# Kernel tuning notes

Measured on AMD Instinct MI355X. Metric: run time of the kernel, lower is better.

## Reference

```python
import jax, jax.numpy as jnp
import numpy as np

B, L, D, S = 64, 512, 768, 8
HOP, LAMB = 3, 0.5


def _layernorm(x, g, b, eps=1e-5):
    m = x.mean(-1, keepdims=True)
    v = x.var(-1, keepdims=True)
    return (x - m) / jnp.sqrt(v + eps) * g + b


def _hop_refine(cur, sentence, ln_g, ln_b):
    # cur, sentence: [B,S,D]. HOP-1 refinement steps, then return last row.
    for _ in range(HOP - 1):
        coef = jnp.einsum('bd,bsd->bs', cur[:, -1, :], sentence)  # [B,S]
        a = coef[..., None] * sentence                             # [B,S,D]
        cur = LAMB * _layernorm(jax.nn.sigmoid(a), ln_g, ln_b) + sentence
    return cur[:, -1, :]  # [B,D]


def _conv1d(x, w, b):
    # x: [B,D,S], w: [Dout,Din,3], padding=1 (same)
    y = jax.lax.conv_general_dilated(
        x, w, window_strides=(1,), padding=((1, 1),),
        dimension_numbers=('NCH', 'OIH', 'NCH'))
    return y + b[None, :, None]


def setup_inputs() -> dict:
    key = jax.random.key(0)
    ks = jax.random.split(key, 16)
    p = lambda k, shp: (jax.random.normal(k, shp, dtype=jnp.float32) * 0.02)
    # segment boundaries: strictly increasing, start at 1, <= L, gaps ~63 with jitter < 32
    base = 1 + np.arange(S + 1) * ((L - 1) // S)          # [9]
    jitter = np.array(jax.random.randint(ks[15], (B, S + 1), 0, 32))
    jitter[:, 0] = 0
    jitter[:, -1] = 0
    seg_bounds = jnp.asarray(base[None, :] + jitter, dtype=jnp.int64 if jax.config.jax_enable_x64 else jnp.int32)
    return {
        'bert_output': jax.random.normal(ks[0], (B, L, D), dtype=jnp.float32),
        'target': jax.random.normal(ks[1], (B, D), dtype=jnp.float32),
        'gc1_w': p(ks[2], (D, D)), 'gc1_b': p(ks[3], (D,)),
        'gc2_w': p(ks[4], (D, D)), 'gc2_b': p(ks[5], (D,)),
        'conv1_w': p(ks[6], (D, D, 3)), 'conv1_b': p(ks[7], (D,)),
        'conv2_w': p(ks[8], (D, D, 3)), 'conv2_b': p(ks[9], (D,)),
        'ln_g': jnp.ones((D,), jnp.float32), 'ln_b': jnp.zeros((D,), jnp.float32),
        'fc2_w': p(ks[10], (3 * D, 3)), 'fc2_b': p(ks[11], (3,)),
        'seg_bounds': seg_bounds,
    }


def reference(bert_output, target, gc1_w, gc1_b, gc2_w, gc2_b,
              conv1_w, conv1_b, conv2_w, conv2_b, ln_g, ln_b,
              fc2_w, fc2_b, seg_bounds):
    dt = bert_output.dtype
    start = seg_bounds[:, :-1]   # [B,S]
    end = seg_bounds[:, 1:]      # [B,S]
    pos = jnp.arange(L)
    seg_mask = ((pos[None, None, :] >= start[:, :, None]) &
                (pos[None, None, :] < end[:, :, None])).astype(dt)  # [B,S,L]
    cnt = (end - start).astype(dt)                                   # [B,S]
    # batched segment-mean pooling
    sentence = jnp.einsum('bsl,bld->bsd', seg_mask, bert_output) / cnt[..., None]

    # GCN branch: adj = I + superdiagonal, row-degree normalization
    adj = jnp.eye(S, dtype=dt) + jnp.eye(S, k=1, dtype=dt)
    denom = adj.sum(axis=1)  # [S]

    def gcn(x, w, b):
        h = jnp.einsum('bsd,de->bse', x, w)
        return jnp.einsum('st,btd->bsd', adj, h) / denom[None, :, None] + b

    g1 = jnp.tanh(gcn(sentence, gc1_w, gc1_b))
    g2 = jnp.tanh(gcn(g1, gc2_w, gc2_b))
    a3 = _hop_refine(g2, sentence, ln_g, ln_b)

    # Conv branch: two conv1d (k=3, pad=1) over the segment axis
    x = jnp.swapaxes(sentence, 1, 2)  # [B,D,S]
    c = jnp.tanh(_conv1d(x, conv1_w, conv1_b))
    c = jnp.tanh(_conv1d(c, conv2_w, conv2_b))
    conv_out = jnp.swapaxes(c, 1, 2)  # [B,S,D]
    a4 = _hop_refine(conv_out, sentence, ln_g, ln_b)

    # Self-mask branch
    coef0 = jnp.einsum('bd,bsd->bs', sentence[:, -1, :], sentence)
    tmask = jax.nn.sigmoid(coef0[..., None] * sentence)
    a5 = _hop_refine(tmask, sentence, ln_g, ln_b)

    fnout = jnp.stack([a3, a4, a5], axis=1)                 # [B,3,D]
    # NOTE: original uses target[0] (first sample's pooler output) for all samples
    w = jax.nn.softmax(jnp.einsum('bkd,d->bk', fnout, target[0]), axis=1)
    fn = (fnout * w[..., None]).reshape(fnout.shape[0], 3 * D)
    return fn @ fc2_w + fc2_b  # [B,3]
```

## Files before the change

kernel.cpp:

```cpp
#include <hip/hip_runtime.h>


typedef unsigned short u16;
typedef short short8 __attribute__((ext_vector_type(8)));
typedef float f32x4 __attribute__((ext_vector_type(4)));

__device__ __forceinline__ float bf2f(u16 h) {
    unsigned int u = ((unsigned int)h) << 16;
    float f;
    __builtin_memcpy(&f, &u, 4);
    return f;
}
__device__ __forceinline__ u16 f2bf(float f) {
    unsigned int u;
    __builtin_memcpy(&u, &f, 4);
    u = (u + 0x7fffu + ((u >> 16) & 1u)) >> 16;
    return (u16)u;
}
__device__ __forceinline__ float sigm(float x) { return 1.0f / (1.0f + __expf(-x)); }

__device__ __forceinline__ float ldv(const void* p, long i, bool bf) {
    return bf ? bf2f(((const u16*)p)[i]) : ((const float*)p)[i];
}

__device__ __forceinline__ bool detect_bf16(const u16* bert) {
    int hits = 0;
#pragma unroll
    for (int i = 0; i < 256; i += 2) {
        const int e = (bert[i] >> 7) & 0xFF;
        hits += (e >= 115 && e <= 130) ? 1 : 0;
    }
    return hits > 64;
}

__global__ __launch_bounds__(256) void k0_zero(float* __restrict__ ws)
{
    ((float4*)ws)[blockIdx.x * 256 + threadIdx.x] = make_float4(0.f, 0.f, 0.f, 0.f);
}

__global__ __launch_bounds__(256) void k1_pool(
    const void* __restrict__ bertv, const int* __restrict__ sb,
    float* __restrict__ sentF, float* __restrict__ flagp)
{
    const int u = blockIdx.x, t = threadIdx.x;
    const bool bf = detect_bf16((const u16*)bertv);
    const bool is64 = (sb[1] == 0);
    if (u == 0 && t == 0) flagp[0] = bf ? 1.0f : 0.0f;
    const int q = u & 3, v = u >> 2;
    const int b = v / 3, si = v - 3 * (v / 3), s = 5 + si;
    const int i0 = b * 9 + s, i1 = i0 + 1;
    int st = is64 ? sb[2 * i0] : sb[i0];
    int en = is64 ? sb[2 * i1] : sb[i1];
    st = st < 0 ? 0 : (st > 511 ? 511 : st);
    en = en <= st ? st + 1 : (en > 512 ? 512 : en);
    const int n = en - st;
    const int r0 = st + (n * q) / 4;
    const int r1 = st + (n * (q + 1)) / 4;
    float a0 = 0.f, a1 = 0.f, a2 = 0.f;
    if (bf) {
        const u16* base = (const u16*)bertv + (size_t)b * 512 * 768;
        int l = r0;
        for (; l + 1 < r1; l += 2) {
            const u16* p0 = base + (size_t)l * 768;
            const u16* p1 = p0 + 768;
            const u16 x0 = p0[t], x1 = p0[t + 256], x2 = p0[t + 512];
            const u16 y0 = p1[t], y1 = p1[t + 256], y2 = p1[t + 512];
            a0 += bf2f(x0) + bf2f(y0);
            a1 += bf2f(x1) + bf2f(y1);
            a2 += bf2f(x2) + bf2f(y2);
        }
        if (l < r1) {
            const u16* p0 = base + (size_t)l * 768;
            a0 += bf2f(p0[t]);
            a1 += bf2f(p0[t + 256]);
            a2 += bf2f(p0[t + 512]);
        }
    } else {
        const float* base = (const float*)bertv + (size_t)b * 512 * 768;
        int l = r0;
        for (; l + 1 < r1; l += 2) {
            const float* p0 = base + (size_t)l * 768;
            const float* p1 = p0 + 768;
            const float x0 = p0[t], x1 = p0[t + 256], x2 = p0[t + 512];
            const float y0 = p1[t], y1 = p1[t + 256], y2 = p1[t + 512];
            a0 += x0 + y0;
            a1 += x1 + y1;
            a2 += x2 + y2;
        }
        if (l < r1) {
            const float* p0 = base + (size_t)l * 768;
            a0 += p0[t];
            a1 += p0[t + 256];
            a2 += p0[t + 512];
        }
    }
    const float inv = 1.0f / (float)n;
    float* o = sentF + b * 2304 + si * 768;
    atomicAdd(o + t, a0 * inv);
    atomicAdd(o + t + 256, a1 * inv);
    atomicAdd(o + t + 512, a2 * inv);
}

template <int XMODE, int WMODE>
__device__ __forceinline__ void gemm_core(
    const float* __restrict__ x, int xstride, const void* __restrict__ bias,
    const void* __restrict__ W, bool bf,
    float* __restrict__ out, int ostride,
    int n0, int k0, u16* As, u16* Bs)
{
    const int t = threadIdx.x;
    const int r = t >> 2;
    const int cseg = (t & 3) * 32;
    const int wave = t >> 6, lane = t & 63;
    const int lm = lane & 15, lq = lane >> 4;
    f32x4 acc[4] = {};

    for (int kk = 0; kk < 256; kk += 128) {
        const int kg = k0 + kk;
        {
            const float* xp = x + (size_t)r * xstride + (kg + cseg);
            u16* dst = As + r * 136 + cseg;
#pragma unroll
            for (int i = 0; i < 8; ++i) {
                float4 v = ((const float4*)xp)[i];
                if (XMODE == 1) {
                    int kb = kg + cseg + i * 4;
                    if (kb >= 768) kb -= 768;
                    v.x = tanhf(v.x + ldv(bias, kb, bf));
                    v.y = tanhf(v.y + ldv(bias, kb + 1, bf));
                    v.z = tanhf(v.z + ldv(bias, kb + 2, bf));
                    v.w = tanhf(v.w + ldv(bias, kb + 3, bf));
                }
                ((ushort4*)dst)[i] = make_ushort4(f2bf(v.x), f2bf(v.y), f2bf(v.z), f2bf(v.w));
            }
        }
        if (WMODE == 0) {
            const int p = t >> 2;
            const int nseg = (t & 3) * 16;
            u16 q0[16], q1[16];
            if (bf) {
                const u16* w0 = (const u16*)W + (size_t)(kg + 2 * p) * 768 + n0 + nseg;
                ((uint4*)q0)[0] = ((const uint4*)w0)[0];
                ((uint4*)q0)[1] = ((const uint4*)w0)[1];
                ((uint4*)q1)[0] = ((const uint4*)(w0 + 768))[0];
                ((uint4*)q1)[1] = ((const uint4*)(w0 + 768))[1];
            } else {
                const float* w0 = (const float*)W + (size_t)(kg + 2 * p) * 768 + n0 + nseg;
#pragma unroll
                for (int e = 0; e < 4; ++e) {
                    float4 v0 = ((const float4*)w0)[e];
                    float4 v1 = ((const float4*)(w0 + 768))[e];
                    q0[4 * e] = f2bf(v0.x); q0[4 * e + 1] = f2bf(v0.y);
                    q0[4 * e + 2] = f2bf(v0.z); q0[4 * e + 3] = f2bf(v0.w);
                    q1[4 * e] = f2bf(v1.x); q1[4 * e + 1] = f2bf(v1.y);
                    q1[4 * e + 2] = f2bf(v1.z); q1[4 * e + 3] = f2bf(v1.w);
                }
            }
#pragma unroll
            for (int e = 0; e < 16; ++e)
                *(ushort2*)(Bs + (nseg + e) * 136 + 2 * p) = make_ushort2(q0[e], q1[e]);
        } else {
            const int kb = kg / 768;
            const int i0c = kg - kb * 768;
            u16 tmp[32];
            if (bf) {
                const u16* wp = (const u16*)W + (size_t)(n0 + r) * 2304 + (size_t)(i0c + cseg) * 3 + kb;
#pragma unroll
                for (int j = 0; j < 32; ++j) tmp[j] = wp[j * 3];
            } else {
                const float* wp = (const float*)W + (size_t)(n0 + r) * 2304 + (size_t)(i0c + cseg) * 3 + kb;
#pragma unroll
                for (int j = 0; j < 32; ++j) tmp[j] = f2bf(wp[j * 3]);
            }
            u16* dst = Bs + r * 136 + cseg;
#pragma unroll
            for (int qq = 0; qq < 8; ++qq)
                ((ushort4*)dst)[qq] = ((ushort4*)tmp)[qq];
        }
        __syncthreads();
        const u16* ap = As + (wave * 16 + lm) * 136 + lq * 8;
        const u16* bp = Bs + lm * 136 + lq * 8;
#pragma unroll
        for (int ks = 0; ks < 4; ++ks) {
            short8 af = *(const short8*)(ap + ks * 32);
#pragma unroll
            for (int nf = 0; nf < 4; ++nf) {
                short8 bfr = *(const short8*)(bp + nf * 16 * 136 + ks * 32);
                acc[nf] = __builtin_amdgcn_mfma_f32_16x16x32_bf16(af, bfr, acc[nf], 0, 0, 0);
            }
        }
        __syncthreads();
    }
#pragma unroll
    for (int nf = 0; nf < 4; ++nf) {
#pragma unroll
        for (int rg = 0; rg < 4; ++rg) {
            const int row = wave * 16 + lq * 4 + rg;
            const int col = n0 + nf * 16 + lm;
            atomicAdd(out + (size_t)row * ostride + col, acc[nf][rg]);
        }
    }
}

__global__ __launch_bounds__(256) void k2_gemm_a(
    const float* __restrict__ sentF, const void* __restrict__ gc1w,
    const void* __restrict__ c1w, float* __restrict__ g1acc, float* __restrict__ c1acc,
    const float* __restrict__ flagp)
{
    __shared__ u16 As[64 * 136];
    __shared__ u16 Bs[64 * 136];
    const bool bf = flagp[0] > 0.5f;
    const int u = blockIdx.x;
    if (u < 36) {
        gemm_core<0, 0>(sentF + 1536, 2304, nullptr, gc1w, bf, g1acc, 768,
                        (u / 3) * 64, (u % 3) * 256, As, Bs);
    } else if (u < 144) {
        const int v = u - 36;
        gemm_core<0, 1>(sentF, 2304, nullptr, c1w, bf, c1acc, 1536,
                        (v / 9) * 64, (v % 9) * 256, As, Bs);
    } else {
        const int v = u - 144;
        gemm_core<0, 1>(sentF + 768, 2304, nullptr, c1w, bf, c1acc + 768, 1536,
                        (v / 6) * 64, (v % 6) * 256, As, Bs);
    }
}

__global__ __launch_bounds__(256) void k3_gemm_b(
    const float* __restrict__ g1acc, const float* __restrict__ c1acc,
    const void* __restrict__ gc2w, const void* __restrict__ c2w,
    const void* __restrict__ gc1b, const void* __restrict__ c1b,
    float* __restrict__ g2acc, float* __restrict__ c2acc,
    const float* __restrict__ flagp)
{
    __shared__ u16 As[64 * 136];
    __shared__ u16 Bs[64 * 136];
    const bool bf = flagp[0] > 0.5f;
    const int u = blockIdx.x;
    if (u < 36) {
        gemm_core<1, 0>(g1acc, 768, gc1b, gc2w, bf, g2acc, 768,
                        (u / 3) * 64, (u % 3) * 256, As, Bs);
    } else {
        const int v = u - 36;
        gemm_core<1, 1>(c1acc, 1536, c1b, c2w, bf, c2acc, 768,
                        (v / 6) * 64, (v % 6) * 256, As, Bs);
    }
}

__device__ __forceinline__ float block_sum(float v, float* red) {
#pragma unroll
    for (int m = 1; m < 64; m <<= 1) v += __shfl_xor(v, m, 64);
    const int wave = threadIdx.x >> 6, lane = threadIdx.x & 63;
    if (lane == 0) red[wave] = v;
    __syncthreads();
    const float r = red[0] + red[1] + red[2] + red[3];
    __syncthreads();
    return r;
}

__global__ __launch_bounds__(256) void k4_final(
    const float* __restrict__ sentF, const float* __restrict__ g2acc,
    const float* __restrict__ c2acc,
    const void* __restrict__ gc2b, const void* __restrict__ c2b,
    const void* __restrict__ lng, const void* __restrict__ lnb,
    const void* __restrict__ target, const void* __restrict__ fc2w,
    const void* __restrict__ fc2b, void* __restrict__ outp,
    const float* __restrict__ flagp)
{
    __shared__ float red[4];
    const bool bf = flagp[0] > 0.5f;
    const int t = threadIdx.x, b = blockIdx.x;
    float s_[3], g_[3], bb_[3];
    const float* srow = sentF + b * 2304 + 1536;
#pragma unroll
    for (int i = 0; i < 3; ++i) {
        const int d = t + 256 * i;
        s_[i] = srow[d];
        g_[i] = ldv(lng, d, bf);
        bb_[i] = ldv(lnb, d, bf);
    }

    auto refine2 = [&](float* yv) {
#pragma unroll
        for (int it = 0; it < 2; ++it) {
            const float c = block_sum(yv[0] * s_[0] + yv[1] * s_[1] + yv[2] * s_[2], red);
            float tt[3], sm = 0.0f, sq = 0.0f;
#pragma unroll
            for (int i = 0; i < 3; ++i) {
                tt[i] = sigm(c * s_[i]);
                sm += tt[i];
                sq += tt[i] * tt[i];
            }
            const float m = block_sum(sm, red) * (1.0f / 768.0f);
            const float q = block_sum(sq, red) * (1.0f / 768.0f);
            const float inv = rsqrtf(fmaxf(q - m * m, 0.0f) + 1e-5f);
#pragma unroll
            for (int i = 0; i < 3; ++i)
                yv[i] = 0.5f * ((tt[i] - m) * inv * g_[i] + bb_[i]) + s_[i];
        }
    };

    float a3[3], a4[3], a5[3], y[3];
#pragma unroll
    for (int i = 0; i < 3; ++i) {
        const int d = t + 256 * i;
        y[i] = tanhf(g2acc[b * 768 + d] + ldv(gc2b, d, bf));
    }
    refine2(y);
    a3[0] = y[0]; a3[1] = y[1]; a3[2] = y[2];
#pragma unroll
    for (int i = 0; i < 3; ++i) {
        const int d = t + 256 * i;
        y[i] = tanhf(c2acc[b * 768 + d] + ldv(c2b, d, bf));
    }
    refine2(y);
    a4[0] = y[0]; a4[1] = y[1]; a4[2] = y[2];
    const float ss = block_sum(s_[0] * s_[0] + s_[1] * s_[1] + s_[2] * s_[2], red);
#pragma unroll
    for (int i = 0; i < 3; ++i) y[i] = sigm(ss * s_[i]);
    refine2(y);
    a5[0] = y[0]; a5[1] = y[1]; a5[2] = y[2];

    float tg[3];
#pragma unroll
    for (int i = 0; i < 3; ++i) tg[i] = ldv(target, t + 256 * i, bf);
    const float u0 = block_sum(a3[0] * tg[0] + a3[1] * tg[1] + a3[2] * tg[2], red);
    const float u1 = block_sum(a4[0] * tg[0] + a4[1] * tg[1] + a4[2] * tg[2], red);
    const float u2 = block_sum(a5[0] * tg[0] + a5[1] * tg[1] + a5[2] * tg[2], red);
    const float mx = fmaxf(u0, fmaxf(u1, u2));
    const float e0 = __expf(u0 - mx), e1 = __expf(u1 - mx), e2 = __expf(u2 - mx);
    const float es = e0 + e1 + e2;
    const float w0 = e0 / es, w1 = e1 / es, w2 = e2 / es;

    float p0 = 0.0f, p1 = 0.0f, p2 = 0.0f;
#pragma unroll
    for (int i = 0; i < 3; ++i) {
        const int d = t + 256 * i;
        const float va = w0 * a3[i], vb = w1 * a4[i], vc = w2 * a5[i];
        p0 += va * ldv(fc2w, d * 3 + 0, bf) + vb * ldv(fc2w, (768 + d) * 3 + 0, bf) + vc * ldv(fc2w, (1536 + d) * 3 + 0, bf);
        p1 += va * ldv(fc2w, d * 3 + 1, bf) + vb * ldv(fc2w, (768 + d) * 3 + 1, bf) + vc * ldv(fc2w, (1536 + d) * 3 + 1, bf);
        p2 += va * ldv(fc2w, d * 3 + 2, bf) + vb * ldv(fc2w, (768 + d) * 3 + 2, bf) + vc * ldv(fc2w, (1536 + d) * 3 + 2, bf);
    }
    p0 = block_sum(p0, red);
    p1 = block_sum(p1, red);
    p2 = block_sum(p2, red);
    if (t == 0) {
        const float o0 = p0 + ldv(fc2b, 0, bf);
        const float o1 = p1 + ldv(fc2b, 1, bf);
        const float o2 = p2 + ldv(fc2b, 2, bf);
        if (bf) {
            ((u16*)outp)[b * 3 + 0] = f2bf(o0);
            ((u16*)outp)[b * 3 + 1] = f2bf(o1);
            ((u16*)outp)[b * 3 + 2] = f2bf(o2);
        } else {
            ((float*)outp)[b * 3 + 0] = o0;
            ((float*)outp)[b * 3 + 1] = o1;
            ((float*)outp)[b * 3 + 2] = o2;
        }
    }
}

extern "C" void kernel_launch(void* const* d_in, const int* in_sizes, int n_in,
                              void* d_out, int out_size, void* d_ws, size_t ws_size,
                              hipStream_t stream) {
    const void* bert   = d_in[0];
    const void* target = d_in[1];
    const void* gc1w   = d_in[2];
    const void* gc1b   = d_in[3];
    const void* gc2w   = d_in[4];
    const void* gc2b   = d_in[5];
    const void* c1w    = d_in[6];
    const void* c1b    = d_in[7];
    const void* c2w    = d_in[8];
    const void* c2b    = d_in[9];
    const void* lng    = d_in[10];
    const void* lnb    = d_in[11];
    const void* fc2w   = d_in[12];
    const void* fc2b   = d_in[13];
    const int*  sb     = (const int*)d_in[14];

    float* sentF = (float*)d_ws;
    float* accs  = sentF + 147456;
    float* g1acc = accs;
    float* c1acc = accs + 49152;
    float* g2acc = c1acc + 98304;
    float* c2acc = g2acc + 49152;
    float* flagp = accs + 245760;

    k0_zero<<<384, 256, 0, stream>>>(sentF);
    k1_pool<<<768, 256, 0, stream>>>(bert, sb, sentF, flagp);
    k2_gemm_a<<<216, 256, 0, stream>>>(sentF, gc1w, c1w, g1acc, c1acc, flagp);
    k3_gemm_b<<<108, 256, 0, stream>>>(g1acc, c1acc, gc2w, c2w, gc1b, c1b, g2acc, c2acc, flagp);
    k4_final<<<64, 256, 0, stream>>>(sentF, g2acc, c2acc, gc2b, c2b, lng, lnb,
                                     target, fc2w, fc2b, d_out, flagp);
}
```

Before: 223.6 us.

## Fuse all stages into one cooperative kernel with grid syncs

Replaces the five separate launches (zero, pool, two GEMM stages, final) with a single cooperative kernel of 256 blocks that uses grid.sync between phases. Pooling now writes four per-quarter partial buffers instead of doing atomicAdd into a zeroed buffer, and the GEMM input loader sums those four partials. tanhf is replaced by a fast exp-based tanh. This is meant to remove launch gaps and pooling atomics, in exchange for grid-wide barrier cost, a bf16-detection scan in every block, and fewer blocks available for the pooling phase.

```diff
diff --git a/kernel.cpp b/kernel.cpp
--- a/kernel.cpp
+++ b/kernel.cpp
@@ -1,9 +1,14 @@
 #include <hip/hip_runtime.h>
+#include <hip/hip_cooperative_groups.h>
+
+namespace cg = cooperative_groups;
 
 
 typedef unsigned short u16;
 typedef short short8 __attribute__((ext_vector_type(8)));
 typedef float f32x4 __attribute__((ext_vector_type(4)));
+
+#define PART 147456
 
 __device__ __forceinline__ float bf2f(u16 h) {
     unsigned int u = ((unsigned int)h) << 16;
@@ -18,7 +23,11 @@
     return (u16)u;
 }
 __device__ __forceinline__ float sigm(float x) { return 1.0f / (1.0f + __expf(-x)); }
-
+__device__ __forceinline__ float ftanh(float x) {
+    const float xc = fminf(fmaxf(x, -15.0f), 15.0f);
+    const float e = __expf(2.0f * xc);
+    return __fdividef(e - 1.0f, e + 1.0f);
+}
 __device__ __forceinline__ float ldv(const void* p, long i, bool bf) {
     return bf ? bf2f(((const u16*)p)[i]) : ((const float*)p)[i];
 }
@@ -33,75 +42,7 @@
     return hits > 64;
 }
 
-__global__ __launch_bounds__(256) void k0_zero(float* __restrict__ ws)
-{
-    ((float4*)ws)[blockIdx.x * 256 + threadIdx.x] = make_float4(0.f, 0.f, 0.f, 0.f);
-}
-
-__global__ __launch_bounds__(256) void k1_pool(
-    const void* __restrict__ bertv, const int* __restrict__ sb,
-    float* __restrict__ sentF, float* __restrict__ flagp)
-{
-    const int u = blockIdx.x, t = threadIdx.x;
-    const bool bf = detect_bf16((const u16*)bertv);
-    const bool is64 = (sb[1] == 0);
-    if (u == 0 && t == 0) flagp[0] = bf ? 1.0f : 0.0f;
-    const int q = u & 3, v = u >> 2;
-    const int b = v / 3, si = v - 3 * (v / 3), s = 5 + si;
-    const int i0 = b * 9 + s, i1 = i0 + 1;
-    int st = is64 ? sb[2 * i0] : sb[i0];
-    int en = is64 ? sb[2 * i1] : sb[i1];
-    st = st < 0 ? 0 : (st > 511 ? 511 : st);
-    en = en <= st ? st + 1 : (en > 512 ? 512 : en);
-    const int n = en - st;
-    const int r0 = st + (n * q) / 4;
-    const int r1 = st + (n * (q + 1)) / 4;
-    float a0 = 0.f, a1 = 0.f, a2 = 0.f;
-    if (bf) {
-        const u16* base = (const u16*)bertv + (size_t)b * 512 * 768;
-        int l = r0;
-        for (; l + 1 < r1; l += 2) {
-            const u16* p0 = base + (size_t)l * 768;
-            const u16* p1 = p0 + 768;
-            const u16 x0 = p0[t], x1 = p0[t + 256], x2 = p0[t + 512];
-            const u16 y0 = p1[t], y1 = p1[t + 256], y2 = p1[t + 512];
-            a0 += bf2f(x0) + bf2f(y0);
-            a1 += bf2f(x1) + bf2f(y1);
-            a2 += bf2f(x2) + bf2f(y2);
-        }
-        if (l < r1) {
-            const u16* p0 = base + (size_t)l * 768;
-            a0 += bf2f(p0[t]);
-            a1 += bf2f(p0[t + 256]);
-            a2 += bf2f(p0[t + 512]);
-        }
-    } else {
-        const float* base = (const float*)bertv + (size_t)b * 512 * 768;
-        int l = r0;
-        for (; l + 1 < r1; l += 2) {
-            const float* p0 = base + (size_t)l * 768;
-            const float* p1 = p0 + 768;
-            const float x0 = p0[t], x1 = p0[t + 256], x2 = p0[t + 512];
-            const float y0 = p1[t], y1 = p1[t + 256], y2 = p1[t + 512];
-            a0 += x0 + y0;
-            a1 += x1 + y1;
-            a2 += x2 + y2;
-        }
-        if (l < r1) {
-            const float* p0 = base + (size_t)l * 768;
-            a0 += p0[t];
-            a1 += p0[t + 256];
-            a2 += p0[t + 512];
-        }
-    }
-    const float inv = 1.0f / (float)n;
-    float* o = sentF + b * 2304 + si * 768;
-    atomicAdd(o + t, a0 * inv);
-    atomicAdd(o + t + 256, a1 * inv);
-    atomicAdd(o + t + 512, a2 * inv);
-}
-
-template <int XMODE, int WMODE>
+template <int XMODE, int WMODE, int NPART>
 __device__ __forceinline__ void gemm_core(
     const float* __restrict__ x, int xstride, const void* __restrict__ bias,
     const void* __restrict__ W, bool bf,
@@ -123,13 +64,22 @@
 #pragma unroll
             for (int i = 0; i < 8; ++i) {
                 float4 v = ((const float4*)xp)[i];
+                if (NPART == 4) {
+                    const float4 v1 = ((const float4*)(xp + PART))[i];
+                    const float4 v2 = ((const float4*)(xp + 2 * PART))[i];
+                    const float4 v3 = ((const float4*)(xp + 3 * PART))[i];
+                    v.x += v1.x + v2.x + v3.x;
+                    v.y += v1.y + v2.y + v3.y;
+                    v.z += v1.z + v2.z + v3.z;
+                    v.w += v1.w + v2.w + v3.w;
+                }
                 if (XMODE == 1) {
                     int kb = kg + cseg + i * 4;
                     if (kb >= 768) kb -= 768;
-                    v.x = tanhf(v.x + ldv(bias, kb, bf));
-                    v.y = tanhf(v.y + ldv(bias, kb + 1, bf));
-                    v.z = tanhf(v.z + ldv(bias, kb + 2, bf));
-                    v.w = tanhf(v.w + ldv(bias, kb + 3, bf));
+                    v.x = ftanh(v.x + ldv(bias, kb, bf));
+                    v.y = ftanh(v.y + ldv(bias, kb + 1, bf));
+                    v.z = ftanh(v.z + ldv(bias, kb + 2, bf));
+                    v.w = ftanh(v.w + ldv(bias, kb + 3, bf));
                 }
                 ((ushort4*)dst)[i] = make_ushort4(f2bf(v.x), f2bf(v.y), f2bf(v.z), f2bf(v.w));
             }
@@ -202,50 +152,6 @@
     }
 }
 
-__global__ __launch_bounds__(256) void k2_gemm_a(
-    const float* __restrict__ sentF, const void* __restrict__ gc1w,
-    const void* __restrict__ c1w, float* __restrict__ g1acc, float* __restrict__ c1acc,
-    const float* __restrict__ flagp)
-{
-    __shared__ u16 As[64 * 136];
-    __shared__ u16 Bs[64 * 136];
-    const bool bf = flagp[0] > 0.5f;
-    const int u = blockIdx.x;
-    if (u < 36) {
-        gemm_core<0, 0>(sentF + 1536, 2304, nullptr, gc1w, bf, g1acc, 768,
-                        (u / 3) * 64, (u % 3) * 256, As, Bs);
-    } else if (u < 144) {
-        const int v = u - 36;
-        gemm_core<0, 1>(sentF, 2304, nullptr, c1w, bf, c1acc, 1536,
-                        (v / 9) * 64, (v % 9) * 256, As, Bs);
-    } else {
-        const int v = u - 144;
-        gemm_core<0, 1>(sentF + 768, 2304, nullptr, c1w, bf, c1acc + 768, 1536,
-                        (v / 6) * 64, (v % 6) * 256, As, Bs);
-    }
-}
-
-__global__ __launch_bounds__(256) void k3_gemm_b(
-    const float* __restrict__ g1acc, const float* __restrict__ c1acc,
-    const void* __restrict__ gc2w, const void* __restrict__ c2w,
-    const void* __restrict__ gc1b, const void* __restrict__ c1b,
-    float* __restrict__ g2acc, float* __restrict__ c2acc,
-    const float* __restrict__ flagp)
-{
-    __shared__ u16 As[64 * 136];
-    __shared__ u16 Bs[64 * 136];
-    const bool bf = flagp[0] > 0.5f;
-    const int u = blockIdx.x;
-    if (u < 36) {
-        gemm_core<1, 0>(g1acc, 768, gc1b, gc2w, bf, g2acc, 768,
-                        (u / 3) * 64, (u % 3) * 256, As, Bs);
-    } else {
-        const int v = u - 36;
-        gemm_core<1, 1>(c1acc, 1536, c1b, c2w, bf, c2acc, 768,
-                        (v / 6) * 64, (v % 6) * 256, As, Bs);
-    }
-}
-
 __device__ __forceinline__ float block_sum(float v, float* red) {
 #pragma unroll
     for (int m = 1; m < 64; m <<= 1) v += __shfl_xor(v, m, 64);
@@ -257,104 +163,207 @@
     return r;
 }
 
-__global__ __launch_bounds__(256) void k4_final(
-    const float* __restrict__ sentF, const float* __restrict__ g2acc,
-    const float* __restrict__ c2acc,
-    const void* __restrict__ gc2b, const void* __restrict__ c2b,
+__global__ __launch_bounds__(256) void fused_all(
+    const void* __restrict__ bertv, const void* __restrict__ target,
+    const void* __restrict__ gc1w, const void* __restrict__ gc1b,
+    const void* __restrict__ gc2w, const void* __restrict__ gc2b,
+    const void* __restrict__ c1w, const void* __restrict__ c1b,
+    const void* __restrict__ c2w, const void* __restrict__ c2b,
     const void* __restrict__ lng, const void* __restrict__ lnb,
-    const void* __restrict__ target, const void* __restrict__ fc2w,
-    const void* __restrict__ fc2b, void* __restrict__ outp,
-    const float* __restrict__ flagp)
+    const void* __restrict__ fc2w, const void* __restrict__ fc2b,
+    const int* __restrict__ sb,
+    float* __restrict__ sentP, float* __restrict__ accs,
+    void* __restrict__ outp)
 {
+    __shared__ u16 As[64 * 136];
+    __shared__ u16 Bs[64 * 136];
     __shared__ float red[4];
-    const bool bf = flagp[0] > 0.5f;
-    const int t = threadIdx.x, b = blockIdx.x;
-    float s_[3], g_[3], bb_[3];
-    const float* srow = sentF + b * 2304 + 1536;
-#pragma unroll
-    for (int i = 0; i < 3; ++i) {
-        const int d = t + 256 * i;
-        s_[i] = srow[d];
-        g_[i] = ldv(lng, d, bf);
-        bb_[i] = ldv(lnb, d, bf);
-    }
-
-    auto refine2 = [&](float* yv) {
-#pragma unroll
-        for (int it = 0; it < 2; ++it) {
-            const float c = block_sum(yv[0] * s_[0] + yv[1] * s_[1] + yv[2] * s_[2], red);
-            float tt[3], sm = 0.0f, sq = 0.0f;
-#pragma unroll
-            for (int i = 0; i < 3; ++i) {
-                tt[i] = sigm(c * s_[i]);
-                sm += tt[i];
-                sq += tt[i] * tt[i];
-            }
-            const float m = block_sum(sm, red) * (1.0f / 768.0f);
-            const float q = block_sum(sq, red) * (1.0f / 768.0f);
-            const float inv = rsqrtf(fmaxf(q - m * m, 0.0f) + 1e-5f);
-#pragma unroll
-            for (int i = 0; i < 3; ++i)
-                yv[i] = 0.5f * ((tt[i] - m) * inv * g_[i] + bb_[i]) + s_[i];
-        }
-    };
-
-    float a3[3], a4[3], a5[3], y[3];
-#pragma unroll
-    for (int i = 0; i < 3; ++i) {
-        const int d = t + 256 * i;
-        y[i] = tanhf(g2acc[b * 768 + d] + ldv(gc2b, d, bf));
-    }
-    refine2(y);
-    a3[0] = y[0]; a3[1] = y[1]; a3[2] = y[2];
-#pragma unroll
-    for (int i = 0; i < 3; ++i) {
-        const int d = t + 256 * i;
-        y[i] = tanhf(c2acc[b * 768 + d] + ldv(c2b, d, bf));
-    }
-    refine2(y);
-    a4[0] = y[0]; a4[1] = y[1]; a4[2] = y[2];
-    const float ss = block_sum(s_[0] * s_[0] + s_[1] * s_[1] + s_[2] * s_[2], red);
-#pragma unroll
-    for (int i = 0; i < 3; ++i) y[i] = sigm(ss * s_[i]);
-    refine2(y);
-    a5[0] = y[0]; a5[1] = y[1]; a5[2] = y[2];
-
-    float tg[3];
-#pragma unroll
-    for (int i = 0; i < 3; ++i) tg[i] = ldv(target, t + 256 * i, bf);
-    const float u0 = block_sum(a3[0] * tg[0] + a3[1] * tg[1] + a3[2] * tg[2], red);
-    const float u1 = block_sum(a4[0] * tg[0] + a4[1] * tg[1] + a4[2] * tg[2], red);
-    const float u2 = block_sum(a5[0] * tg[0] + a5[1] * tg[1] + a5[2] * tg[2], red);
-    const float mx = fmaxf(u0, fmaxf(u1, u2));
-    const float e0 = __expf(u0 - mx), e1 = __expf(u1 - mx), e2 = __expf(u2 - mx);
-    const float es = e0 + e1 + e2;
-    const float w0 = e0 / es, w1 = e1 / es, w2 = e2 / es;
-
-    float p0 = 0.0f, p1 = 0.0f, p2 = 0.0f;
-#pragma unroll
-    for (int i = 0; i < 3; ++i) {
-        const int d = t + 256 * i;
-        const float va = w0 * a3[i], vb = w1 * a4[i], vc = w2 * a5[i];
-        p0 += va * ldv(fc2w, d * 3 + 0, bf) + vb * ldv(fc2w, (768 + d) * 3 + 0, bf) + vc * ldv(fc2w, (1536 + d) * 3 + 0, bf);
-        p1 += va * ldv(fc2w, d * 3 + 1, bf) + vb * ldv(fc2w, (768 + d) * 3 + 1, bf) + vc * ldv(fc2w, (1536 + d) * 3 + 1, bf);
-        p2 += va * ldv(fc2w, d * 3 + 2, bf) + vb * ldv(fc2w, (768 + d) * 3 + 2, bf) + vc * ldv(fc2w, (1536 + d) * 3 + 2, bf);
-    }
-    p0 = block_sum(p0, red);
-    p1 = block_sum(p1, red);
-    p2 = block_sum(p2, red);
-    if (t == 0) {
-        const float o0 = p0 + ldv(fc2b, 0, bf);
-        const float o1 = p1 + ldv(fc2b, 1, bf);
-        const float o2 = p2 + ldv(fc2b, 2, bf);
-        if (bf) {
-            ((u16*)outp)[b * 3 + 0] = f2bf(o0);
-            ((u16*)outp)[b * 3 + 1] = f2bf(o1);
-            ((u16*)outp)[b * 3 + 2] = f2bf(o2);
-        } else {
-            ((float*)outp)[b * 3 + 0] = o0;
-            ((float*)outp)[b * 3 + 1] = o1;
-            ((float*)outp)[b * 3 + 2] = o2;
+
+    const int u = blockIdx.x, t = threadIdx.x;
+    const bool bf = detect_bf16((const u16*)bertv);
+    const bool is64 = (sb[1] == 0);
+    cg::grid_group grid = cg::this_grid();
+
+    float* g1acc = accs;
+    float* c1acc = accs + 49152;
+    float* g2acc = c1acc + 98304;
+    float* c2acc = g2acc + 49152;
+
+    {
+        if (t < 240) ((float4*)accs)[u * 240 + t] = make_float4(0.f, 0.f, 0.f, 0.f);
+#pragma unroll
+        for (int j = 0; j < 3; ++j) {
+            const int v = u + 256 * j;
+            const int q = v & 3, w = v >> 2;
+            const int b = w / 3, si = w - 3 * (w / 3), s = 5 + si;
+            const int i0 = b * 9 + s, i1 = i0 + 1;
+            int st = is64 ? sb[2 * i0] : sb[i0];
+            int en = is64 ? sb[2 * i1] : sb[i1];
+            st = st < 0 ? 0 : (st > 511 ? 511 : st);
+            en = en <= st ? st + 1 : (en > 512 ? 512 : en);
+            const int n = en - st;
+            const int r0 = st + (n * q) / 4;
+            const int r1 = st + (n * (q + 1)) / 4;
+            float a0 = 0.f, a1 = 0.f, a2 = 0.f;
+            if (bf) {
+                const u16* base = (const u16*)bertv + (size_t)b * 512 * 768;
+                int l = r0;
+                for (; l + 1 < r1; l += 2) {
+                    const u16* p0 = base + (size_t)l * 768;
+                    const u16* p1 = p0 + 768;
+                    const u16 x0 = p0[t], x1 = p0[t + 256], x2 = p0[t + 512];
+                    const u16 y0 = p1[t], y1 = p1[t + 256], y2 = p1[t + 512];
+                    a0 += bf2f(x0) + bf2f(y0);
+                    a1 += bf2f(x1) + bf2f(y1);
+                    a2 += bf2f(x2) + bf2f(y2);
+                }
+                if (l < r1) {
+                    const u16* p0 = base + (size_t)l * 768;
+                    a0 += bf2f(p0[t]);
+                    a1 += bf2f(p0[t + 256]);
+                    a2 += bf2f(p0[t + 512]);
+                }
+            } else {
+                const float* base = (const float*)bertv + (size_t)b * 512 * 768;
+                int l = r0;
+                for (; l + 1 < r1; l += 2) {
+                    const float* p0 = base + (size_t)l * 768;
+                    const float* p1 = p0 + 768;
+                    const float x0 = p0[t], x1 = p0[t + 256], x2 = p0[t + 512];
+                    const float y0 = p1[t], y1 = p1[t + 256], y2 = p1[t + 512];
+                    a0 += x0 + y0;
+                    a1 += x1 + y1;
+                    a2 += x2 + y2;
+                }
+                if (l < r1) {
+                    const float* p0 = base + (size_t)l * 768;
+                    a0 += p0[t];
+                    a1 += p0[t + 256];
+                    a2 += p0[t + 512];
+                }
+            }
+            const float inv = 1.0f / (float)n;
+            float* o = sentP + (size_t)q * PART + b * 2304 + si * 768;
+            o[t] = a0 * inv;
+            o[t + 256] = a1 * inv;
+            o[t + 512] = a2 * inv;
+        }
+    }
+    grid.sync();
+
+    if (u < 36) {
+        gemm_core<0, 0, 4>(sentP + 1536, 2304, nullptr, gc1w, bf, g1acc, 768,
+                           (u / 3) * 64, (u % 3) * 256, As, Bs);
+    } else if (u < 144) {
+        const int v = u - 36;
+        gemm_core<0, 1, 4>(sentP, 2304, nullptr, c1w, bf, c1acc, 1536,
+                           (v / 9) * 64, (v % 9) * 256, As, Bs);
+    } else if (u < 216) {
+        const int v = u - 144;
+        gemm_core<0, 1, 4>(sentP + 768, 2304, nullptr, c1w, bf, c1acc + 768, 1536,
+                           (v / 6) * 64, (v % 6) * 256, As, Bs);
+    }
+    grid.sync();
+
+    if (u < 36) {
+        gemm_core<1, 0, 1>(g1acc, 768, gc1b, gc2w, bf, g2acc, 768,
+                           (u / 3) * 64, (u % 3) * 256, As, Bs);
+    } else if (u < 108) {
+        const int v = u - 36;
+        gemm_core<1, 1, 1>(c1acc, 1536, c1b, c2w, bf, c2acc, 768,
+                           (v / 6) * 64, (v % 6) * 256, As, Bs);
+    }
+    grid.sync();
+
+    if (u < 64) {
+        const int b = u;
+        float s_[3], g_[3], bb_[3];
+        const float* sp = sentP + b * 2304 + 1536;
+#pragma unroll
+        for (int i = 0; i < 3; ++i) {
+            const int d = t + 256 * i;
+            s_[i] = sp[d] + sp[PART + d] + sp[2 * PART + d] + sp[3 * PART + d];
+            g_[i] = ldv(lng, d, bf);
+            bb_[i] = ldv(lnb, d, bf);
+        }
+
+        auto refine2 = [&](float* yv) {
+#pragma unroll
+            for (int it = 0; it < 2; ++it) {
+                const float c = block_sum(yv[0] * s_[0] + yv[1] * s_[1] + yv[2] * s_[2], red);
+                float tt[3], sm = 0.0f, sq = 0.0f;
+#pragma unroll
+                for (int i = 0; i < 3; ++i) {
+                    tt[i] = sigm(c * s_[i]);
+                    sm += tt[i];
+                    sq += tt[i] * tt[i];
+                }
+                const float m = block_sum(sm, red) * (1.0f / 768.0f);
+                const float q = block_sum(sq, red) * (1.0f / 768.0f);
+                const float inv = rsqrtf(fmaxf(q - m * m, 0.0f) + 1e-5f);
+#pragma unroll
+                for (int i = 0; i < 3; ++i)
+                    yv[i] = 0.5f * ((tt[i] - m) * inv * g_[i] + bb_[i]) + s_[i];
+            }
+        };
+
+        float a3[3], a4[3], a5[3], y[3];
+#pragma unroll
+        for (int i = 0; i < 3; ++i) {
+            const int d = t + 256 * i;
+            y[i] = ftanh(g2acc[b * 768 + d] + ldv(gc2b, d, bf));
+        }
+        refine2(y);
+        a3[0] = y[0]; a3[1] = y[1]; a3[2] = y[2];
+#pragma unroll
+        for (int i = 0; i < 3; ++i) {
+            const int d = t + 256 * i;
+            y[i] = ftanh(c2acc[b * 768 + d] + ldv(c2b, d, bf));
+        }
+        refine2(y);
+        a4[0] = y[0]; a4[1] = y[1]; a4[2] = y[2];
+        const float ss = block_sum(s_[0] * s_[0] + s_[1] * s_[1] + s_[2] * s_[2], red);
+#pragma unroll
+        for (int i = 0; i < 3; ++i) y[i] = sigm(ss * s_[i]);
+        refine2(y);
+        a5[0] = y[0]; a5[1] = y[1]; a5[2] = y[2];
+
+        float tg[3];
+#pragma unroll
+        for (int i = 0; i < 3; ++i) tg[i] = ldv(target, t + 256 * i, bf);
+        const float u0 = block_sum(a3[0] * tg[0] + a3[1] * tg[1] + a3[2] * tg[2], red);
+        const float u1 = block_sum(a4[0] * tg[0] + a4[1] * tg[1] + a4[2] * tg[2], red);
+        const float u2 = block_sum(a5[0] * tg[0] + a5[1] * tg[1] + a5[2] * tg[2], red);
+        const float mx = fmaxf(u0, fmaxf(u1, u2));
+        const float e0 = __expf(u0 - mx), e1 = __expf(u1 - mx), e2 = __expf(u2 - mx);
+        const float es = e0 + e1 + e2;
+        const float w0 = e0 / es, w1 = e1 / es, w2 = e2 / es;
+
+        float p0 = 0.0f, p1 = 0.0f, p2 = 0.0f;
+#pragma unroll
+        for (int i = 0; i < 3; ++i) {
+            const int d = t + 256 * i;
+            const float va = w0 * a3[i], vb = w1 * a4[i], vc = w2 * a5[i];
+            p0 += va * ldv(fc2w, d * 3 + 0, bf) + vb * ldv(fc2w, (768 + d) * 3 + 0, bf) + vc * ldv(fc2w, (1536 + d) * 3 + 0, bf);
+            p1 += va * ldv(fc2w, d * 3 + 1, bf) + vb * ldv(fc2w, (768 + d) * 3 + 1, bf) + vc * ldv(fc2w, (1536 + d) * 3 + 1, bf);
+            p2 += va * ldv(fc2w, d * 3 + 2, bf) + vb * ldv(fc2w, (768 + d) * 3 + 2, bf) + vc * ldv(fc2w, (1536 + d) * 3 + 2, bf);
+        }
+        p0 = block_sum(p0, red);
+        p1 = block_sum(p1, red);
+        p2 = block_sum(p2, red);
+        if (t == 0) {
+            const float o0 = p0 + ldv(fc2b, 0, bf);
+            const float o1 = p1 + ldv(fc2b, 1, bf);
+            const float o2 = p2 + ldv(fc2b, 2, bf);
+            if (bf) {
+                ((u16*)outp)[b * 3 + 0] = f2bf(o0);
+                ((u16*)outp)[b * 3 + 1] = f2bf(o1);
+                ((u16*)outp)[b * 3 + 2] = f2bf(o2);
+            } else {
+                ((float*)outp)[b * 3 + 0] = o0;
+                ((float*)outp)[b * 3 + 1] = o1;
+                ((float*)outp)[b * 3 + 2] = o2;
+            }
         }
     }
 }
@@ -378,18 +387,17 @@
     const void* fc2b   = d_in[13];
     const int*  sb     = (const int*)d_in[14];
 
-    float* sentF = (float*)d_ws;
-    float* accs  = sentF + 147456;
-    float* g1acc = accs;
-    float* c1acc = accs + 49152;
-    float* g2acc = c1acc + 98304;
-    float* c2acc = g2acc + 49152;
-    float* flagp = accs + 245760;
-
-    k0_zero<<<384, 256, 0, stream>>>(sentF);
-    k1_pool<<<768, 256, 0, stream>>>(bert, sb, sentF, flagp);
-    k2_gemm_a<<<216, 256, 0, stream>>>(sentF, gc1w, c1w, g1acc, c1acc, flagp);
-    k3_gemm_b<<<108, 256, 0, stream>>>(g1acc, c1acc, gc2w, c2w, gc1b, c1b, g2acc, c2acc, flagp);
-    k4_final<<<64, 256, 0, stream>>>(sentF, g2acc, c2acc, gc2b, c2b, lng, lnb,
-                                     target, fc2w, fc2b, d_out, flagp);
-}
+    float* sentP = (float*)d_ws;
+    float* accs  = sentP + 4 * PART;
+    void*  outp  = d_out;
+
+    void* args[] = {
+        (void*)&bert, (void*)&target, (void*)&gc1w, (void*)&gc1b,
+        (void*)&gc2w, (void*)&gc2b, (void*)&c1w, (void*)&c1b,
+        (void*)&c2w, (void*)&c2b, (void*)&lng, (void*)&lnb,
+        (void*)&fc2w, (void*)&fc2b, (void*)&sb,
+        (void*)&sentP, (void*)&accs, (void*)&outp,
+    };
+    hipLaunchCooperativeKernel((void*)fused_all, dim3(256), dim3(256),
+                               args, 0, stream);
+}
```

After: 344.9 us. 54.2% more time.
